# Kernel tuning notes

Hardware: AMD Instinct MI355X
Metric: run time of the kernel (lower is better)

Reference implementation:

```python
import jax, jax.numpy as jnp
import numpy as np


def _maxpool2(x):
    # 2x2 max pool, stride 2, NCHW
    return jax.lax.reduce_window(x, -jnp.inf, jax.lax.max, (1, 1, 2, 2), (1, 1, 2, 2), 'VALID')


def _up2(x):
    # bilinear upsample x2 with align_corners=True (matches nn.Upsample), NCHW, separable
    def rs(a, axis):
        n = a.shape[axis]
        out = 2 * n
        c = jnp.arange(out) * ((n - 1) / (out - 1))
        i0 = jnp.floor(c).astype(jnp.int32)
        i1 = jnp.minimum(i0 + 1, n - 1)
        w = (c - i0).astype(a.dtype)
        lo = jnp.take(a, i0, axis=axis)
        hi = jnp.take(a, i1, axis=axis)
        shp = [1] * a.ndim
        shp[axis] = out
        w = w.reshape(shp)
        return lo * (1 - w) + hi * w
    return rs(rs(x, 2), 3)


def _conv_experts(x, w, b):
    # x [B,Cin,H,W], w [E,Cout,Cin,3,3], b [E,Cout] -> [E,B,Cout,H,W]
    def one(we, be):
        y = jax.lax.conv_general_dilated(x, we, (1, 1), 'SAME',
                                         dimension_numbers=('NCHW', 'OIHW', 'NCHW'))
        return jax.nn.relu(y + be[None, :, None, None])
    return jax.vmap(one)(w, b)


def _moe(x, cw, cb, gw, gb, nw, nb, eps, k):
    # noisy top-k gate (create_gate) + fused gated expert sum (eval_gate)
    B = x.shape[0]
    xf = x.reshape(B, -1)
    g = xf @ gw + gb                      # [B,E]
    noise = jax.nn.softplus(xf @ nw + nb)
    g = g + eps[None, :] * noise          # shared per-expert gaussian noise * per-sample scale
    E = g.shape[1]
    if E > 2:
        _, idx = jax.lax.top_k(g.sum(axis=0), k)   # top-k experts by batch-summed gate
        mask = jnp.zeros((E,), bool).at[idx].set(True)
        g = jnp.where(mask[None, :], g, 0.0)       # zero BEFORE softmax, as in the original
    gate = jax.nn.softmax(g, axis=-1)
    y = _conv_experts(x, cw, cb)          # [E,B,C,H,W]
    # collapses the original experts x batch python double-loop into one contraction
    return jnp.einsum('ebchw,be->bchw', y, gate)


def setup_inputs():
    key = jax.random.key(0)
    keys = iter(jax.random.split(key, 40))
    def rn(shape, scale=1.0):
        return jax.random.normal(next(keys), shape, jnp.float32) * scale
    B, W, E = 2048, 10, 4
    inp = {'x': rn((B, 1, 28, 28))}
    conv_shapes = [(E, W, 1, 3, 3), (E, W, W, 3, 3), (E, 2 * W, W, 3, 3),
                   (E, W, 3 * W, 3, 3), (E, W, 2 * W, 3, 3)]
    gate_in = [784, 1960, 490, 5880, 15680]
    for i in range(5):
        inp[f'cw{i+1}'] = rn(conv_shapes[i], 0.1)
        inp[f'cb{i+1}'] = rn((E, conv_shapes[i][1]), 0.1)
        inp[f'gw{i+1}'] = rn((gate_in[i], E), 0.02)
        inp[f'gb{i+1}'] = rn((E,), 0.02)
        inp[f'nw{i+1}'] = rn((gate_in[i], E), 0.02)
        inp[f'nb{i+1}'] = rn((E,), 0.02)
        inp[f'eps{i+1}'] = rn((E,), 1.0)   # N(mu=0, sigma=1) gate noise, fixed for determinism
    inp['wlast'] = rn((1, W, 1, 1), 0.1)
    inp['blast'] = rn((1,), 0.1)
    inp['k'] = 2
    return inp


def reference(x, cw1, cb1, gw1, gb1, nw1, nb1, eps1,
              cw2, cb2, gw2, gb2, nw2, nb2, eps2,
              cw3, cb3, gw3, gb3, nw3, nb3, eps3,
              cw4, cb4, gw4, gb4, nw4, nb4, eps4,
              cw5, cb5, gw5, gb5, nw5, nb5, eps5,
              wlast, blast, k):
    conv1 = _moe(x, cw1, cb1, gw1, gb1, nw1, nb1, eps1, k)        # [B,10,28,28]
    h = _maxpool2(conv1)                                          # [B,10,14,14]
    conv2 = _moe(h, cw2, cb2, gw2, gb2, nw2, nb2, eps2, k)        # [B,10,14,14]
    h = _maxpool2(conv2)                                          # [B,10,7,7]
    conv3 = _moe(h, cw3, cb3, gw3, gb3, nw3, nb3, eps3, k)        # [B,20,7,7]
    h = jnp.concatenate([_up2(conv3), conv2], axis=1)             # [B,30,14,14]
    h = _moe(h, cw4, cb4, gw4, gb4, nw4, nb4, eps4, k)            # [B,10,14,14]
    h = jnp.concatenate([_up2(h), conv1], axis=1)                 # [B,20,28,28]
    h = _moe(h, cw5, cb5, gw5, gb5, nw5, nb5, eps5, k)            # [B,10,28,28]
    out = jnp.einsum('bchw,oc->bohw', h, wlast[:, :, 0, 0]) + blast[None, :, None, None]
    return out
```

## Files before the change

### kernel.cpp

```cpp
#include <hip/hip_runtime.h>
#include <hip/hip_bf16.h>
#include <math.h>


constexpr int BATCH = 2048;

constexpr size_t PADF    = 1024;
constexpr size_t F_CONV1 = (size_t)BATCH * 10 * 784;
constexpr size_t F_XPAD  = (size_t)BATCH * 784;
constexpr size_t F_P1    = (size_t)BATCH * 10 * 196;
constexpr size_t F_CONV2 = F_P1;
constexpr size_t F_P2    = (size_t)BATCH * 10 * 49;
constexpr size_t F_CONV3 = (size_t)BATCH * 20 * 49;
constexpr size_t F_UP3   = (size_t)BATCH * 20 * 196;
constexpr size_t F_M4    = F_P1;
constexpr size_t F_UP4   = F_CONV1;

constexpr size_t O_CONV1 = PADF;
constexpr size_t O_Z2    = O_CONV1 + F_CONV1 + PADF;
constexpr size_t O_XPAD  = O_Z2;
constexpr size_t O_P1    = O_XPAD + F_XPAD + PADF;
constexpr size_t O_CONV2 = O_P1 + F_P1 + PADF;
constexpr size_t O_P2    = O_CONV2 + F_CONV2 + PADF;
constexpr size_t O_CONV3 = O_P2 + F_P2 + PADF;
constexpr size_t O_UP3   = O_CONV3 + F_CONV3 + PADF;
constexpr size_t O_M4    = O_UP3 + F_UP3 + PADF;
constexpr size_t O_UP4   = O_Z2;
constexpr size_t O_GRAW  = O_M4 + F_M4 + PADF;
constexpr size_t O_CS    = O_GRAW + 5 * (size_t)BATCH * 4;
constexpr size_t WS_FLOATS = O_CS + 5 * 64 + PADF;

__device__ __forceinline__ float softplusf(float z) {
    return fmaxf(z, 0.0f) + log1pf(expf(-fabsf(z)));
}

__device__ __forceinline__ float4 ld4(const float* p) {
    return *(const float4*)p;
}

constexpr int cdivc(int a, int b) { return (a + b - 1) / b; }
constexpr int pb4(int H, int W) {
    return cdivc(BATCH * ((H + 3) / 4) * W, 256);
}

template <int C1HW, int C2HW>
__global__ __launch_bounds__(256) void gate_block_v4(
    const float* __restrict__ x1, const float* __restrict__ x2,
    const float* __restrict__ gw, const float* __restrict__ gb,
    const float* __restrict__ nw, const float* __restrict__ nb,
    const float* __restrict__ eps,
    float* __restrict__ graw)
{
    constexpr int DV = (C1HW + C2HW) / 4;
    const int b   = blockIdx.x;
    const int tid = threadIdx.x;

    float ga0 = 0.f, ga1 = 0.f, ga2 = 0.f, ga3 = 0.f;
    float na0 = 0.f, na1 = 0.f, na2 = 0.f, na3 = 0.f;

    for (int g = tid; g < DV; g += 256) {
        const int d = g * 4;
        float4 xv;
        if constexpr (C2HW > 0) {
            xv = (d < C1HW) ? ld4(x1 + (size_t)b * C1HW + d)
                            : ld4(x2 + (size_t)b * C2HW + (d - C1HW));
        } else {
            xv = ld4(x1 + (size_t)b * C1HW + d);
        }
        const float xs[4] = {xv.x, xv.y, xv.z, xv.w};
        #pragma unroll
        for (int j = 0; j < 4; ++j) {
            const float val = xs[j];
            const float4 gv = ((const float4*)gw)[d + j];
            const float4 nv = ((const float4*)nw)[d + j];
            ga0 = fmaf(val, gv.x, ga0); ga1 = fmaf(val, gv.y, ga1);
            ga2 = fmaf(val, gv.z, ga2); ga3 = fmaf(val, gv.w, ga3);
            na0 = fmaf(val, nv.x, na0); na1 = fmaf(val, nv.y, na1);
            na2 = fmaf(val, nv.z, na2); na3 = fmaf(val, nv.w, na3);
        }
    }
    #pragma unroll
    for (int m = 32; m >= 1; m >>= 1) {
        ga0 += __shfl_xor(ga0, m, 64); ga1 += __shfl_xor(ga1, m, 64);
        ga2 += __shfl_xor(ga2, m, 64); ga3 += __shfl_xor(ga3, m, 64);
        na0 += __shfl_xor(na0, m, 64); na1 += __shfl_xor(na1, m, 64);
        na2 += __shfl_xor(na2, m, 64); na3 += __shfl_xor(na3, m, 64);
    }
    __shared__ float red[4][8];
    const int wave = tid >> 6, lane = tid & 63;
    if (lane == 0) {
        red[wave][0] = ga0; red[wave][1] = ga1; red[wave][2] = ga2; red[wave][3] = ga3;
        red[wave][4] = na0; red[wave][5] = na1; red[wave][6] = na2; red[wave][7] = na3;
    }
    __syncthreads();
    if (tid == 0) {
        float G[8];
        #pragma unroll
        for (int i = 0; i < 8; ++i)
            G[i] = red[0][i] + red[1][i] + red[2][i] + red[3][i];
        #pragma unroll
        for (int e = 0; e < 4; ++e) {
            graw[b * 4 + e] = G[e] + gb[e] + eps[e] * softplusf(G[4 + e] + nb[e]);
        }
    }
}

template <int D>
__global__ __launch_bounds__(256) void gate_block_s(
    const float* __restrict__ x1,
    const float* __restrict__ gw, const float* __restrict__ gb,
    const float* __restrict__ nw, const float* __restrict__ nb,
    const float* __restrict__ eps,
    float* __restrict__ graw)
{
    const int b   = blockIdx.x;
    const int tid = threadIdx.x;

    float ga0 = 0.f, ga1 = 0.f, ga2 = 0.f, ga3 = 0.f;
    float na0 = 0.f, na1 = 0.f, na2 = 0.f, na3 = 0.f;

    for (int d = tid; d < D; d += 256) {
        const float val = x1[(size_t)b * D + d];
        const float4 gv = ((const float4*)gw)[d];
        const float4 nv = ((const float4*)nw)[d];
        ga0 = fmaf(val, gv.x, ga0); ga1 = fmaf(val, gv.y, ga1);
        ga2 = fmaf(val, gv.z, ga2); ga3 = fmaf(val, gv.w, ga3);
        na0 = fmaf(val, nv.x, na0); na1 = fmaf(val, nv.y, na1);
        na2 = fmaf(val, nv.z, na2); na3 = fmaf(val, nv.w, na3);
    }
    #pragma unroll
    for (int m = 32; m >= 1; m >>= 1) {
        ga0 += __shfl_xor(ga0, m, 64); ga1 += __shfl_xor(ga1, m, 64);
        ga2 += __shfl_xor(ga2, m, 64); ga3 += __shfl_xor(ga3, m, 64);
        na0 += __shfl_xor(na0, m, 64); na1 += __shfl_xor(na1, m, 64);
        na2 += __shfl_xor(na2, m, 64); na3 += __shfl_xor(na3, m, 64);
    }
    __shared__ float red[4][8];
    const int wave = tid >> 6, lane = tid & 63;
    if (lane == 0) {
        red[wave][0] = ga0; red[wave][1] = ga1; red[wave][2] = ga2; red[wave][3] = ga3;
        red[wave][4] = na0; red[wave][5] = na1; red[wave][6] = na2; red[wave][7] = na3;
    }
    __syncthreads();
    if (tid == 0) {
        float G[8];
        #pragma unroll
        for (int i = 0; i < 8; ++i)
            G[i] = red[0][i] + red[1][i] + red[2][i] + red[3][i];
        #pragma unroll
        for (int e = 0; e < 4; ++e) {
            graw[b * 4 + e] = G[e] + gb[e] + eps[e] * softplusf(G[4 + e] + nb[e]);
        }
    }
}

__global__ __launch_bounds__(256) void gate_reduce(
    const float* __restrict__ graw, float* __restrict__ cs)
{
    const int tid = threadIdx.x;
    float a0 = 0.f, a1 = 0.f, a2 = 0.f, a3 = 0.f;
    for (int b = tid; b < BATCH; b += 256) {
        const float4 v = ld4(graw + b * 4);
        a0 += v.x; a1 += v.y; a2 += v.z; a3 += v.w;
    }
    #pragma unroll
    for (int m = 32; m >= 1; m >>= 1) {
        a0 += __shfl_xor(a0, m, 64); a1 += __shfl_xor(a1, m, 64);
        a2 += __shfl_xor(a2, m, 64); a3 += __shfl_xor(a3, m, 64);
    }
    __shared__ float red[4][4];
    const int wave = tid >> 6, lane = tid & 63;
    if (lane == 0) {
        red[wave][0] = a0; red[wave][1] = a1; red[wave][2] = a2; red[wave][3] = a3;
    }
    __syncthreads();
    if (tid < 4) {
        cs[tid] = red[0][tid] + red[1][tid] + red[2][tid] + red[3][tid];
    }
}

template <int CIN1, int CIN2, int COUT, int H, int W, int POOL, int FINAL>
__global__ __launch_bounds__(256) void moe_conv4(
    const float* __restrict__ x1, const float* __restrict__ x2,
    const float* __restrict__ cw, const float* __restrict__ cb,
    const float* __restrict__ graw, const float* __restrict__ colsum,
    const int* __restrict__ kp,
    float* __restrict__ out, float* __restrict__ pout,
    const float* __restrict__ wl, const float* __restrict__ bl)
{
    constexpr int CIN = CIN1 + CIN2;
    constexpr int CG  = 2;
    constexpr int NCG = COUT / CG;
    constexpr int HG  = (H + 3) / 4;
    constexpr int TOTAL = BATCH * HG * W;

    __shared__ __align__(16) float wlds[CIN * 72];

    const unsigned bid = blockIdx.x;
    const unsigned xcd = bid & 7u;
    const unsigned sub = bid >> 3;
    const unsigned cg  = sub % NCG;
    const unsigned tl  = sub / NCG;
    const unsigned tile = tl * 8u + xcd;
    const int c0 = (int)cg * CG;

    for (int idx = threadIdx.x; idx < CIN * 72; idx += 256) {
        const int ci = idx / 72;
        const int r  = idx % 72;
        const int k  = r / 8;
        const int je = r % 8;
        wlds[idx] = cw[((size_t)((je & 3) * COUT + c0 + (je >> 2)) * CIN + ci) * 9 + k];
    }
    __syncthreads();

    const int t = (int)tile * 256 + (int)threadIdx.x;
    if (t >= TOTAL) return;
    const int b  = t / (HG * W);
    const int r  = t - b * (HG * W);
    const int hg = r / W;
    const int w  = r - hg * W;
    const int h0 = hg * 4;

    float gt[4];
    {
        int k = kp[0];
        k = (k < 1) ? 1 : (k > 4 ? 4 : k);
        float cs[4], gr[4];
        bool sel[4] = {false, false, false, false};
        #pragma unroll
        for (int e = 0; e < 4; ++e) { cs[e] = colsum[e]; gr[e] = graw[b * 4 + e]; }
        for (int it = 0; it < k; ++it) {
            int bi = 0; float bv = -INFINITY;
            #pragma unroll
            for (int e = 0; e < 4; ++e)
                if (!sel[e] && cs[e] > bv) { bv = cs[e]; bi = e; }
            sel[bi] = true;
        }
        float g[4];
        #pragma unroll
        for (int e = 0; e < 4; ++e) g[e] = sel[e] ? gr[e] : 0.0f;
        const float mx = fmaxf(fmaxf(g[0], g[1]), fmaxf(g[2], g[3]));
        const float e0 = expf(g[0] - mx), e1 = expf(g[1] - mx);
        const float e2 = expf(g[2] - mx), e3 = expf(g[3] - mx);
        const float inv = 1.0f / (e0 + e1 + e2 + e3);
        gt[0] = e0 * inv; gt[1] = e1 * inv; gt[2] = e2 * inv; gt[3] = e3 * inv;
    }

    float m[6][3];
    #pragma unroll
    for (int rr = 0; rr < 6; ++rr) {
        const int y = h0 - 1 + rr;
        const float my = (y >= 0 && y < H) ? 1.0f : 0.0f;
        #pragma unroll
        for (int dc = 0; dc < 3; ++dc) {
            const int xx = w - 1 + dc;
            m[rr][dc] = ((xx >= 0 && xx < W) ? 1.0f : 0.0f) * my;
        }
    }
    const int base = (h0 - 1) * W + (w - 1);

    float acc[4][CG][4];
    #pragma unroll
    for (int j = 0; j < CG; ++j) {
        #pragma unroll
        for (int e = 0; e < 4; ++e) {
            const float bv = cb[e * COUT + c0 + j];
            #pragma unroll
            for (int rr = 0; rr < 4; ++rr) acc[rr][j][e] = bv;
        }
    }

    const float* xb1 = x1 + (size_t)b * CIN1 * (H * W);
    const float* xb2 = (CIN2 > 0) ? (x2 + (size_t)b * CIN2 * (H * W)) : nullptr;

    auto xplane = [&](int ci) -> const float* {
        if constexpr (CIN2 > 0)
            return (ci < CIN1) ? (xb1 + ci * (H * W)) : (xb2 + (ci - CIN1) * (H * W));
        else
            return xb1 + ci * (H * W);
    };
    auto load_taps = [&](int ci, float v[6][3]) {
        const float* xp = xplane(ci);
        #pragma unroll
        for (int rr = 0; rr < 6; ++rr)
            #pragma unroll
            for (int dc = 0; dc < 3; ++dc)
                v[rr][dc] = xp[base + rr * W + dc];
    };
    auto fma_taps = [&](int ci, const float v[6][3]) {
        float mv[6][3];
        #pragma unroll
        for (int rr = 0; rr < 6; ++rr)
            #pragma unroll
            for (int dc = 0; dc < 3; ++dc)
                mv[rr][dc] = v[rr][dc] * m[rr][dc];
        const float4* wp = (const float4*)&wlds[ci * 72];
        #pragma unroll
        for (int k = 0; k < 9; ++k) {
            const float4 wA = wp[k * 2];
            const float4 wB = wp[k * 2 + 1];
            const int kh = k / 3, kw = k % 3;
            #pragma unroll
            for (int rr = 0; rr < 4; ++rr) {
                const float tap = mv[rr + kh][kw];
                acc[rr][0][0] = fmaf(tap, wA.x, acc[rr][0][0]);
                acc[rr][0][1] = fmaf(tap, wA.y, acc[rr][0][1]);
                acc[rr][0][2] = fmaf(tap, wA.z, acc[rr][0][2]);
                acc[rr][0][3] = fmaf(tap, wA.w, acc[rr][0][3]);
                acc[rr][1][0] = fmaf(tap, wB.x, acc[rr][1][0]);
                acc[rr][1][1] = fmaf(tap, wB.y, acc[rr][1][1]);
                acc[rr][1][2] = fmaf(tap, wB.z, acc[rr][1][2]);
                acc[rr][1][3] = fmaf(tap, wB.w, acc[rr][1][3]);
            }
        }
    };

    float vA[6][3], vB[6][3];
    load_taps(0, vA);
    #pragma unroll 1
    for (int ci = 0; ci + 2 <= CIN; ci += 2) {
        load_taps(ci + 1, vB);
        fma_taps(ci, vA);
        if (ci + 2 < CIN) load_taps(ci + 2, vA);
        fma_taps(ci + 1, vB);
    }
    if constexpr (CIN & 1) {
        fma_taps(CIN - 1, vA);
    }

    float s[4][CG];
    #pragma unroll
    for (int rr = 0; rr < 4; ++rr)
        #pragma unroll
        for (int j = 0; j < CG; ++j)
            s[rr][j] = gt[0] * fmaxf(acc[rr][j][0], 0.f)
                     + gt[1] * fmaxf(acc[rr][j][1], 0.f)
                     + gt[2] * fmaxf(acc[rr][j][2], 0.f)
                     + gt[3] * fmaxf(acc[rr][j][3], 0.f);

    if constexpr (FINAL) {
        const float w0 = wl[c0], w1 = wl[c0 + 1];
        const float bshare = bl[0] * (1.0f / (float)NCG);
        float* op = out + (size_t)b * (H * W) + h0 * W + w;
        #pragma unroll
        for (int rr = 0; rr < 4; ++rr) {
            if (h0 + rr < H)
                atomicAdd(&op[rr * W], s[rr][0] * w0 + s[rr][1] * w1 + bshare);
        }
    } else {
        #pragma unroll
        for (int j = 0; j < CG; ++j) {
            float* op = out + ((size_t)b * COUT + c0 + j) * (H * W) + h0 * W + w;
            #pragma unroll
            for (int rr = 0; rr < 4; ++rr)
                if (h0 + rr < H) op[rr * W] = s[rr][j];
        }
    }

    if constexpr (POOL) {
        constexpr int H2 = H / 2, W2 = W / 2;
        #pragma unroll
        for (int j = 0; j < CG; ++j) {
            float cm0 = fmaxf(s[0][j], s[1][j]);
            float cm1 = fmaxf(s[2][j], s[3][j]);
            const float o0 = fmaxf(cm0, __shfl_xor(cm0, 1, 64));
            const float o1 = fmaxf(cm1, __shfl_xor(cm1, 1, 64));
            if ((w & 1) == 0) {
                const int pr0 = h0 >> 1;
                float* pp = pout + ((size_t)b * COUT + c0 + j) * (H2 * W2) + (w >> 1);
                if (pr0     < H2) pp[pr0 * W2]       = o0;
                if (pr0 + 1 < H2) pp[(pr0 + 1) * W2] = o1;
            }
        }
    }
}

template <int N>
__global__ __launch_bounds__(256) void upsample2(
    const float* __restrict__ in, float* __restrict__ out, int BC)
{
    constexpr int M = 2 * N;
    const int idx = blockIdx.x * 256 + threadIdx.x;
    const int total = BC * M * M;
    if (idx >= total) return;
    const int x = idx % M;
    int tmp = idx / M;
    const int y = tmp % M;
    const int bc = tmp / M;
    const float scale = (float)((double)(N - 1) / (double)(M - 1));
    const float cy = (float)y * scale;
    const float cx = (float)x * scale;
    const int iy0 = (int)floorf(cy);
    const int ix0 = (int)floorf(cx);
    const int iy1 = min(iy0 + 1, N - 1);
    const int ix1 = min(ix0 + 1, N - 1);
    const float wy = cy - (float)iy0;
    const float wx = cx - (float)ix0;
    const float* p = in + (size_t)bc * N * N;
    const float v00 = p[iy0 * N + ix0], v01 = p[iy0 * N + ix1];
    const float v10 = p[iy1 * N + ix0], v11 = p[iy1 * N + ix1];
    const float a0 = v00 * (1.0f - wy) + v10 * wy;
    const float a1 = v01 * (1.0f - wy) + v11 * wy;
    out[idx] = a0 * (1.0f - wx) + a1 * wx;
}

extern "C" void kernel_launch(void* const* d_in, const int* in_sizes, int n_in,
                              void* d_out, int out_size, void* d_ws, size_t ws_size,
                              hipStream_t stream)
{
    const float* x = (const float*)d_in[0];
    const float* cw[5]; const float* cb[5]; const float* gw[5]; const float* gb[5];
    const float* nw[5]; const float* nb[5]; const float* epsv[5];
    for (int l = 0; l < 5; ++l) {
        cw[l]   = (const float*)d_in[1 + 7 * l + 0];
        cb[l]   = (const float*)d_in[1 + 7 * l + 1];
        gw[l]   = (const float*)d_in[1 + 7 * l + 2];
        gb[l]   = (const float*)d_in[1 + 7 * l + 3];
        nw[l]   = (const float*)d_in[1 + 7 * l + 4];
        nb[l]   = (const float*)d_in[1 + 7 * l + 5];
        epsv[l] = (const float*)d_in[1 + 7 * l + 6];
    }
    const float* wlast = (const float*)d_in[36];
    const float* blast = (const float*)d_in[37];
    const int*   kp    = (const int*)d_in[38];
    float* out = (float*)d_out;
    float* ws  = (float*)d_ws;

    float* conv1 = ws + O_CONV1;
    float* xpad  = ws + O_XPAD;
    float* p1    = ws + O_P1;
    float* conv2 = ws + O_CONV2;
    float* p2    = ws + O_P2;
    float* conv3 = ws + O_CONV3;
    float* up3   = ws + O_UP3;
    float* m4    = ws + O_M4;
    float* up4   = ws + O_UP4;
    float* graw[5]; float* cs[5];
    for (int l = 0; l < 5; ++l) {
        graw[l] = ws + O_GRAW + (size_t)l * BATCH * 4;
        cs[l]   = ws + O_CS + (size_t)l * 64;
    }

    hipMemsetAsync(out, 0, (size_t)out_size * sizeof(float), stream);
    hipMemcpyAsync(xpad, x, (size_t)BATCH * 784 * sizeof(float),
                   hipMemcpyDeviceToDevice, stream);

    #define CDIV(a) (((a) + 255) / 256)
    const int g1 = pb4(28, 28) * 5;
    const int g2 = pb4(14, 14) * 5;
    const int g3 = pb4(7, 7)   * 10;
    const int g4 = pb4(14, 14) * 5;
    const int g5 = pb4(28, 28) * 5;

    gate_block_v4<784, 0><<<BATCH, 256, 0, stream>>>(
        x, nullptr, gw[0], gb[0], nw[0], nb[0], epsv[0], graw[0]);
    gate_reduce<<<1, 256, 0, stream>>>(graw[0], cs[0]);
    moe_conv4<1, 0, 10, 28, 28, 1, 0><<<g1, 256, 0, stream>>>(
        xpad, nullptr, cw[0], cb[0], graw[0], cs[0], kp, conv1, p1,
        nullptr, nullptr);

    gate_block_v4<1960, 0><<<BATCH, 256, 0, stream>>>(
        p1, nullptr, gw[1], gb[1], nw[1], nb[1], epsv[1], graw[1]);
    gate_reduce<<<1, 256, 0, stream>>>(graw[1], cs[1]);
    moe_conv4<10, 0, 10, 14, 14, 1, 0><<<g2, 256, 0, stream>>>(
        p1, nullptr, cw[1], cb[1], graw[1], cs[1], kp, conv2, p2,
        nullptr, nullptr);

    gate_block_s<490><<<BATCH, 256, 0, stream>>>(
        p2, gw[2], gb[2], nw[2], nb[2], epsv[2], graw[2]);
    gate_reduce<<<1, 256, 0, stream>>>(graw[2], cs[2]);
    moe_conv4<10, 0, 20, 7, 7, 0, 0><<<g3, 256, 0, stream>>>(
        p2, nullptr, cw[2], cb[2], graw[2], cs[2], kp, conv3, nullptr,
        nullptr, nullptr);
    upsample2<7><<<CDIV(BATCH * 20 * 196), 256, 0, stream>>>(conv3, up3, BATCH * 20);

    gate_block_v4<3920, 1960><<<BATCH, 256, 0, stream>>>(
        up3, conv2, gw[3], gb[3], nw[3], nb[3], epsv[3], graw[3]);
    gate_reduce<<<1, 256, 0, stream>>>(graw[3], cs[3]);
    moe_conv4<20, 10, 10, 14, 14, 0, 0><<<g4, 256, 0, stream>>>(
        up3, conv2, cw[3], cb[3], graw[3], cs[3], kp, m4, nullptr,
        nullptr, nullptr);
    upsample2<14><<<CDIV(BATCH * 10 * 784), 256, 0, stream>>>(m4, up4, BATCH * 10);

    gate_block_v4<7840, 7840><<<BATCH, 256, 0, stream>>>(
        up4, conv1, gw[4], gb[4], nw[4], nb[4], epsv[4], graw[4]);
    gate_reduce<<<1, 256, 0, stream>>>(graw[4], cs[4]);
    moe_conv4<10, 10, 10, 28, 28, 0, 1><<<g5, 256, 0, stream>>>(
        up4, conv1, cw[4], cb[4], graw[4], cs[4], kp, out, nullptr,
        wlast, blast);
    #undef CDIV
}
```

Baseline: 871.3 us.

## Add 2x4 register-tiled conv kernel for 28x28 layers and two-sample gate blocks

Adds a new moe_conv_q4 kernel for the 28x28 layers (conv1 and conv5). Each thread computes a 2-row by 4-column output patch from vectorized float4 row loads, double-buffers input channels, and writes results and the fused 2x2 pool as float4/float2 stores. The old kernel had each thread compute a 4x1 column. The gate GEMV blocks now process two samples per block so the gw/nw weight loads are shared, and the launch grid is halved. The new tile relies on the xpad/workspace padding for out-of-range halo reads and uses more registers, which may lower occupancy.

Measured after the change: 829.2 us. -4.8%, faster.

```diff
diff --git a/kernel.cpp b/kernel.cpp
--- a/kernel.cpp
+++ b/kernel.cpp
@@ -52,55 +52,73 @@
     float* __restrict__ graw)
 {
     constexpr int DV = (C1HW + C2HW) / 4;
-    const int b   = blockIdx.x;
+    const int b0  = blockIdx.x * 2;
     const int tid = threadIdx.x;
 
-    float ga0 = 0.f, ga1 = 0.f, ga2 = 0.f, ga3 = 0.f;
-    float na0 = 0.f, na1 = 0.f, na2 = 0.f, na3 = 0.f;
+    float ga[2][4] = {}, na[2][4] = {};
 
     for (int g = tid; g < DV; g += 256) {
         const int d = g * 4;
-        float4 xv;
-        if constexpr (C2HW > 0) {
-            xv = (d < C1HW) ? ld4(x1 + (size_t)b * C1HW + d)
-                            : ld4(x2 + (size_t)b * C2HW + (d - C1HW));
-        } else {
-            xv = ld4(x1 + (size_t)b * C1HW + d);
-        }
-        const float xs[4] = {xv.x, xv.y, xv.z, xv.w};
+        float4 xv[2];
+        #pragma unroll
+        for (int ss = 0; ss < 2; ++ss) {
+            const int b = b0 + ss;
+            if constexpr (C2HW > 0) {
+                xv[ss] = (d < C1HW) ? ld4(x1 + (size_t)b * C1HW + d)
+                                    : ld4(x2 + (size_t)b * C2HW + (d - C1HW));
+            } else {
+                xv[ss] = ld4(x1 + (size_t)b * C1HW + d);
+            }
+        }
         #pragma unroll
         for (int j = 0; j < 4; ++j) {
-            const float val = xs[j];
             const float4 gv = ((const float4*)gw)[d + j];
             const float4 nv = ((const float4*)nw)[d + j];
-            ga0 = fmaf(val, gv.x, ga0); ga1 = fmaf(val, gv.y, ga1);
-            ga2 = fmaf(val, gv.z, ga2); ga3 = fmaf(val, gv.w, ga3);
-            na0 = fmaf(val, nv.x, na0); na1 = fmaf(val, nv.y, na1);
-            na2 = fmaf(val, nv.z, na2); na3 = fmaf(val, nv.w, na3);
+            #pragma unroll
+            for (int ss = 0; ss < 2; ++ss) {
+                const float val = (&xv[ss].x)[j];
+                ga[ss][0] = fmaf(val, gv.x, ga[ss][0]);
+                ga[ss][1] = fmaf(val, gv.y, ga[ss][1]);
+                ga[ss][2] = fmaf(val, gv.z, ga[ss][2]);
+                ga[ss][3] = fmaf(val, gv.w, ga[ss][3]);
+                na[ss][0] = fmaf(val, nv.x, na[ss][0]);
+                na[ss][1] = fmaf(val, nv.y, na[ss][1]);
+                na[ss][2] = fmaf(val, nv.z, na[ss][2]);
+                na[ss][3] = fmaf(val, nv.w, na[ss][3]);
+            }
         }
     }
     #pragma unroll
     for (int m = 32; m >= 1; m >>= 1) {
-        ga0 += __shfl_xor(ga0, m, 64); ga1 += __shfl_xor(ga1, m, 64);
-        ga2 += __shfl_xor(ga2, m, 64); ga3 += __shfl_xor(ga3, m, 64);
-        na0 += __shfl_xor(na0, m, 64); na1 += __shfl_xor(na1, m, 64);
-        na2 += __shfl_xor(na2, m, 64); na3 += __shfl_xor(na3, m, 64);
-    }
-    __shared__ float red[4][8];
+        #pragma unroll
+        for (int ss = 0; ss < 2; ++ss)
+            #pragma unroll
+            for (int e = 0; e < 4; ++e) {
+                ga[ss][e] += __shfl_xor(ga[ss][e], m, 64);
+                na[ss][e] += __shfl_xor(na[ss][e], m, 64);
+            }
+    }
+    __shared__ float red[4][16];
     const int wave = tid >> 6, lane = tid & 63;
     if (lane == 0) {
-        red[wave][0] = ga0; red[wave][1] = ga1; red[wave][2] = ga2; red[wave][3] = ga3;
-        red[wave][4] = na0; red[wave][5] = na1; red[wave][6] = na2; red[wave][7] = na3;
+        #pragma unroll
+        for (int ss = 0; ss < 2; ++ss)
+            #pragma unroll
+            for (int e = 0; e < 4; ++e) {
+                red[wave][ss * 8 + e]     = ga[ss][e];
+                red[wave][ss * 8 + 4 + e] = na[ss][e];
+            }
     }
     __syncthreads();
-    if (tid == 0) {
-        float G[8];
-        #pragma unroll
-        for (int i = 0; i < 8; ++i)
-            G[i] = red[0][i] + red[1][i] + red[2][i] + red[3][i];
+    if (tid < 2) {
+        const int ss = tid;
         #pragma unroll
         for (int e = 0; e < 4; ++e) {
-            graw[b * 4 + e] = G[e] + gb[e] + eps[e] * softplusf(G[4 + e] + nb[e]);
+            const float G = red[0][ss*8+e] + red[1][ss*8+e]
+                          + red[2][ss*8+e] + red[3][ss*8+e];
+            const float N = red[0][ss*8+4+e] + red[1][ss*8+4+e]
+                          + red[2][ss*8+4+e] + red[3][ss*8+4+e];
+            graw[(b0 + ss) * 4 + e] = G + gb[e] + eps[e] * softplusf(N + nb[e]);
         }
     }
 }
@@ -179,8 +197,35 @@
     }
 }
 
-template <int CIN1, int CIN2, int COUT, int H, int W, int POOL, int FINAL>
-__global__ __launch_bounds__(256) void moe_conv4(
+__device__ __forceinline__ void gate_final(
+    const float* __restrict__ graw, const float* __restrict__ colsum,
+    const int* __restrict__ kp, int b, float gt[4])
+{
+    float cs[4], gr[4];
+    #pragma unroll
+    for (int e = 0; e < 4; ++e) { cs[e] = colsum[e]; gr[e] = graw[b * 4 + e]; }
+    int k = kp[0];
+    k = (k < 1) ? 1 : (k > 4 ? 4 : k);
+    bool sel[4] = {false, false, false, false};
+    for (int it = 0; it < k; ++it) {
+        int bi = 0; float bv = -INFINITY;
+        #pragma unroll
+        for (int e = 0; e < 4; ++e)
+            if (!sel[e] && cs[e] > bv) { bv = cs[e]; bi = e; }
+        sel[bi] = true;
+    }
+    float g[4];
+    #pragma unroll
+    for (int e = 0; e < 4; ++e) g[e] = sel[e] ? gr[e] : 0.0f;
+    const float mx = fmaxf(fmaxf(g[0], g[1]), fmaxf(g[2], g[3]));
+    const float e0 = expf(g[0] - mx), e1 = expf(g[1] - mx);
+    const float e2 = expf(g[2] - mx), e3 = expf(g[3] - mx);
+    const float inv = 1.0f / (e0 + e1 + e2 + e3);
+    gt[0] = e0 * inv; gt[1] = e1 * inv; gt[2] = e2 * inv; gt[3] = e3 * inv;
+}
+
+template <int CIN1, int CIN2, int COUT, int POOL, int FINAL>
+__global__ __launch_bounds__(256) void moe_conv_q4(
     const float* __restrict__ x1, const float* __restrict__ x2,
     const float* __restrict__ cw, const float* __restrict__ cb,
     const float* __restrict__ graw, const float* __restrict__ colsum,
@@ -188,11 +233,11 @@
     float* __restrict__ out, float* __restrict__ pout,
     const float* __restrict__ wl, const float* __restrict__ bl)
 {
+    constexpr int H = 28, W = 28;
     constexpr int CIN = CIN1 + CIN2;
     constexpr int CG  = 2;
     constexpr int NCG = COUT / CG;
-    constexpr int HG  = (H + 3) / 4;
-    constexpr int TOTAL = BATCH * HG * W;
+    constexpr int TOTAL = BATCH * 14 * 7;
 
     __shared__ __align__(16) float wlds[CIN * 72];
 
@@ -215,6 +260,186 @@
 
     const int t = (int)tile * 256 + (int)threadIdx.x;
     if (t >= TOTAL) return;
+    const int b  = t / 98;
+    const int r  = t - b * 98;
+    const int hh = r / 7;
+    const int q  = r - hh * 7;
+    const int h0 = 2 * hh;
+    const int w0 = 4 * q;
+
+    float gt[4];
+    gate_final(graw, colsum, kp, b, gt);
+
+    const float rt = (h0 > 0)      ? 1.0f : 0.0f;
+    const float rb = (h0 + 2 < H)  ? 1.0f : 0.0f;
+    const float cl = (w0 > 0)      ? 1.0f : 0.0f;
+    const float cr = (w0 + 4 < W)  ? 1.0f : 0.0f;
+
+    float acc[2][4][CG][4];
+    #pragma unroll
+    for (int j = 0; j < CG; ++j) {
+        #pragma unroll
+        for (int e = 0; e < 4; ++e) {
+            const float bv = cb[e * COUT + c0 + j];
+            #pragma unroll
+            for (int rr = 0; rr < 2; ++rr)
+                #pragma unroll
+                for (int p = 0; p < 4; ++p) acc[rr][p][j][e] = bv;
+        }
+    }
+
+    const int rbase = (h0 - 1) * W + w0;
+    const float* xb1 = x1 + (size_t)b * CIN1 * (H * W);
+    const float* xb2 = (CIN2 > 0) ? (x2 + (size_t)b * CIN2 * (H * W)) : nullptr;
+
+    auto xplane = [&](int ci) -> const float* {
+        if constexpr (CIN2 > 0)
+            return (ci < CIN1) ? (xb1 + ci * (H * W)) : (xb2 + (ci - CIN1) * (H * W));
+        else
+            return xb1 + ci * (H * W);
+    };
+    auto load_taps = [&](int ci, float v[4][6]) {
+        const float* rp = xplane(ci) + rbase;
+        #pragma unroll
+        for (int rr = 0; rr < 4; ++rr) {
+            const float4 c = ld4(rp + rr * W);
+            v[rr][0] = rp[rr * W - 1];
+            v[rr][1] = c.x; v[rr][2] = c.y; v[rr][3] = c.z; v[rr][4] = c.w;
+            v[rr][5] = rp[rr * W + 4];
+        }
+    };
+    auto fma_taps = [&](int ci, const float v[4][6]) {
+        float mv[4][6];
+        #pragma unroll
+        for (int rr = 0; rr < 4; ++rr) {
+            #pragma unroll
+            for (int c = 0; c < 6; ++c) mv[rr][c] = v[rr][c];
+            mv[rr][0] *= cl;
+            mv[rr][5] *= cr;
+        }
+        #pragma unroll
+        for (int c = 0; c < 6; ++c) { mv[0][c] *= rt; mv[3][c] *= rb; }
+
+        const float4* wp = (const float4*)&wlds[ci * 72];
+        #pragma unroll
+        for (int k = 0; k < 9; ++k) {
+            const float4 wA = wp[k * 2];
+            const float4 wB = wp[k * 2 + 1];
+            const int kh = k / 3, kw = k % 3;
+            #pragma unroll
+            for (int rr = 0; rr < 2; ++rr) {
+                #pragma unroll
+                for (int p = 0; p < 4; ++p) {
+                    const float tap = mv[rr + kh][p + kw];
+                    acc[rr][p][0][0] = fmaf(tap, wA.x, acc[rr][p][0][0]);
+                    acc[rr][p][0][1] = fmaf(tap, wA.y, acc[rr][p][0][1]);
+                    acc[rr][p][0][2] = fmaf(tap, wA.z, acc[rr][p][0][2]);
+                    acc[rr][p][0][3] = fmaf(tap, wA.w, acc[rr][p][0][3]);
+                    acc[rr][p][1][0] = fmaf(tap, wB.x, acc[rr][p][1][0]);
+                    acc[rr][p][1][1] = fmaf(tap, wB.y, acc[rr][p][1][1]);
+                    acc[rr][p][1][2] = fmaf(tap, wB.z, acc[rr][p][1][2]);
+                    acc[rr][p][1][3] = fmaf(tap, wB.w, acc[rr][p][1][3]);
+                }
+            }
+        }
+    };
+
+    float vA[4][6], vB[4][6];
+    load_taps(0, vA);
+    #pragma unroll 1
+    for (int ci = 0; ci + 2 <= CIN; ci += 2) {
+        load_taps(ci + 1, vB);
+        fma_taps(ci, vA);
+        if (ci + 2 < CIN) load_taps(ci + 2, vA);
+        fma_taps(ci + 1, vB);
+    }
+    if constexpr (CIN & 1) {
+        fma_taps(CIN - 1, vA);
+    }
+
+    float s[2][4][CG];
+    #pragma unroll
+    for (int rr = 0; rr < 2; ++rr)
+        #pragma unroll
+        for (int p = 0; p < 4; ++p)
+            #pragma unroll
+            for (int j = 0; j < CG; ++j)
+                s[rr][p][j] = gt[0] * fmaxf(acc[rr][p][j][0], 0.f)
+                            + gt[1] * fmaxf(acc[rr][p][j][1], 0.f)
+                            + gt[2] * fmaxf(acc[rr][p][j][2], 0.f)
+                            + gt[3] * fmaxf(acc[rr][p][j][3], 0.f);
+
+    if constexpr (FINAL) {
+        const float w0f = wl[c0], w1f = wl[c0 + 1];
+        const float bshare = bl[0] * (1.0f / (float)NCG);
+        float* op = out + (size_t)b * (H * W) + h0 * W + w0;
+        #pragma unroll
+        for (int rr = 0; rr < 2; ++rr)
+            #pragma unroll
+            for (int p = 0; p < 4; ++p)
+                atomicAdd(&op[rr * W + p],
+                          s[rr][p][0] * w0f + s[rr][p][1] * w1f + bshare);
+    } else {
+        #pragma unroll
+        for (int j = 0; j < CG; ++j) {
+            float* op = out + ((size_t)b * COUT + c0 + j) * (H * W) + h0 * W + w0;
+            #pragma unroll
+            for (int rr = 0; rr < 2; ++rr) {
+                float4 o = {s[rr][0][j], s[rr][1][j], s[rr][2][j], s[rr][3][j]};
+                *(float4*)(op + rr * W) = o;
+            }
+        }
+    }
+
+    if constexpr (POOL) {
+        constexpr int H2 = 14, W2 = 14;
+        #pragma unroll
+        for (int j = 0; j < CG; ++j) {
+            float2 o;
+            o.x = fmaxf(fmaxf(s[0][0][j], s[0][1][j]), fmaxf(s[1][0][j], s[1][1][j]));
+            o.y = fmaxf(fmaxf(s[0][2][j], s[0][3][j]), fmaxf(s[1][2][j], s[1][3][j]));
+            float* pp = pout + ((size_t)b * COUT + c0 + j) * (H2 * W2)
+                        + hh * W2 + (w0 >> 1);
+            *(float2*)pp = o;
+        }
+    }
+}
+
+template <int CIN1, int CIN2, int COUT, int H, int W, int POOL>
+__global__ __launch_bounds__(256) void moe_conv4(
+    const float* __restrict__ x1, const float* __restrict__ x2,
+    const float* __restrict__ cw, const float* __restrict__ cb,
+    const float* __restrict__ graw, const float* __restrict__ colsum,
+    const int* __restrict__ kp,
+    float* __restrict__ out, float* __restrict__ pout)
+{
+    constexpr int CIN = CIN1 + CIN2;
+    constexpr int CG  = 2;
+    constexpr int NCG = COUT / CG;
+    constexpr int HG  = (H + 3) / 4;
+    constexpr int TOTAL = BATCH * HG * W;
+
+    __shared__ __align__(16) float wlds[CIN * 72];
+
+    const unsigned bid = blockIdx.x;
+    const unsigned xcd = bid & 7u;
+    const unsigned sub = bid >> 3;
+    const unsigned cg  = sub % NCG;
+    const unsigned tl  = sub / NCG;
+    const unsigned tile = tl * 8u + xcd;
+    const int c0 = (int)cg * CG;
+
+    for (int idx = threadIdx.x; idx < CIN * 72; idx += 256) {
+        const int ci = idx / 72;
+        const int r  = idx % 72;
+        const int k  = r / 8;
+        const int je = r % 8;
+        wlds[idx] = cw[((size_t)((je & 3) * COUT + c0 + (je >> 2)) * CIN + ci) * 9 + k];
+    }
+    __syncthreads();
+
+    const int t = (int)tile * 256 + (int)threadIdx.x;
+    if (t >= TOTAL) return;
     const int b  = t / (HG * W);
     const int r  = t - b * (HG * W);
     const int hg = r / W;
@@ -222,29 +447,7 @@
     const int h0 = hg * 4;
 
     float gt[4];
-    {
-        int k = kp[0];
-        k = (k < 1) ? 1 : (k > 4 ? 4 : k);
-        float cs[4], gr[4];
-        bool sel[4] = {false, false, false, false};
-        #pragma unroll
-        for (int e = 0; e < 4; ++e) { cs[e] = colsum[e]; gr[e] = graw[b * 4 + e]; }
-        for (int it = 0; it < k; ++it) {
-            int bi = 0; float bv = -INFINITY;
-            #pragma unroll
-            for (int e = 0; e < 4; ++e)
-                if (!sel[e] && cs[e] > bv) { bv = cs[e]; bi = e; }
-            sel[bi] = true;
-        }
-        float g[4];
-        #pragma unroll
-        for (int e = 0; e < 4; ++e) g[e] = sel[e] ? gr[e] : 0.0f;
-        const float mx = fmaxf(fmaxf(g[0], g[1]), fmaxf(g[2], g[3]));
-        const float e0 = expf(g[0] - mx), e1 = expf(g[1] - mx);
-        const float e2 = expf(g[2] - mx), e3 = expf(g[3] - mx);
-        const float inv = 1.0f / (e0 + e1 + e2 + e3);
-        gt[0] = e0 * inv; gt[1] = e1 * inv; gt[2] = e2 * inv; gt[3] = e3 * inv;
-    }
+    gate_final(graw, colsum, kp, b, gt);
 
     float m[6][3];
     #pragma unroll
@@ -338,23 +541,12 @@
                      + gt[2] * fmaxf(acc[rr][j][2], 0.f)
                      + gt[3] * fmaxf(acc[rr][j][3], 0.f);
 
-    if constexpr (FINAL) {
-        const float w0 = wl[c0], w1 = wl[c0 + 1];
-        const float bshare = bl[0] * (1.0f / (float)NCG);
-        float* op = out + (size_t)b * (H * W) + h0 * W + w;
-        #pragma unroll
-        for (int rr = 0; rr < 4; ++rr) {
-            if (h0 + rr < H)
-                atomicAdd(&op[rr * W], s[rr][0] * w0 + s[rr][1] * w1 + bshare);
-        }
-    } else {
-        #pragma unroll
-        for (int j = 0; j < CG; ++j) {
-            float* op = out + ((size_t)b * COUT + c0 + j) * (H * W) + h0 * W + w;
-            #pragma unroll
-            for (int rr = 0; rr < 4; ++rr)
-                if (h0 + rr < H) op[rr * W] = s[rr][j];
-        }
+    #pragma unroll
+    for (int j = 0; j < CG; ++j) {
+        float* op = out + ((size_t)b * COUT + c0 + j) * (H * W) + h0 * W + w;
+        #pragma unroll
+        for (int rr = 0; rr < 4; ++rr)
+            if (h0 + rr < H) op[rr * W] = s[rr][j];
     }
 
     if constexpr (POOL) {
@@ -446,46 +638,43 @@
                    hipMemcpyDeviceToDevice, stream);
 
     #define CDIV(a) (((a) + 255) / 256)
-    const int g1 = pb4(28, 28) * 5;
-    const int g2 = pb4(14, 14) * 5;
-    const int g3 = pb4(7, 7)   * 10;
-    const int g4 = pb4(14, 14) * 5;
-    const int g5 = pb4(28, 28) * 5;
-
-    gate_block_v4<784, 0><<<BATCH, 256, 0, stream>>>(
+    const int gq  = 784 * 5;
+    const int g2  = pb4(14, 14) * 5;
+    const int g3  = pb4(7, 7)   * 10;
+    const int g4  = pb4(14, 14) * 5;
+    const int GB2 = BATCH / 2;
+
+    gate_block_v4<784, 0><<<GB2, 256, 0, stream>>>(
         x, nullptr, gw[0], gb[0], nw[0], nb[0], epsv[0], graw[0]);
     gate_reduce<<<1, 256, 0, stream>>>(graw[0], cs[0]);
-    moe_conv4<1, 0, 10, 28, 28, 1, 0><<<g1, 256, 0, stream>>>(
+    moe_conv_q4<1, 0, 10, 1, 0><<<gq, 256, 0, stream>>>(
         xpad, nullptr, cw[0], cb[0], graw[0], cs[0], kp, conv1, p1,
         nullptr, nullptr);
 
-    gate_block_v4<1960, 0><<<BATCH, 256, 0, stream>>>(
+    gate_block_v4<1960, 0><<<GB2, 256, 0, stream>>>(
         p1, nullptr, gw[1], gb[1], nw[1], nb[1], epsv[1], graw[1]);
     gate_reduce<<<1, 256, 0, stream>>>(graw[1], cs[1]);
-    moe_conv4<10, 0, 10, 14, 14, 1, 0><<<g2, 256, 0, stream>>>(
-        p1, nullptr, cw[1], cb[1], graw[1], cs[1], kp, conv2, p2,
-        nullptr, nullptr);
+    moe_conv4<10, 0, 10, 14, 14, 1><<<g2, 256, 0, stream>>>(
+        p1, nullptr, cw[1], cb[1], graw[1], cs[1], kp, conv2, p2);
 
     gate_block_s<490><<<BATCH, 256, 0, stream>>>(
         p2, gw[2], gb[2], nw[2], nb[2], epsv[2], graw[2]);
     gate_reduce<<<1, 256, 0, stream>>>(graw[2], cs[2]);
-    moe_conv4<10, 0, 20, 7, 7, 0, 0><<<g3, 256, 0, stream>>>(
-        p2, nullptr, cw[2], cb[2], graw[2], cs[2], kp, conv3, nullptr,
-        nullptr, nullptr);
+    moe_conv4<10, 0, 20, 7, 7, 0><<<g3, 256, 0, stream>>>(
+        p2, nullptr, cw[2], cb[2], graw[2], cs[2], kp, conv3, nullptr);
     upsample2<7><<<CDIV(BATCH * 20 * 196), 256, 0, stream>>>(conv3, up3, BATCH * 20);
 
-    gate_block_v4<3920, 1960><<<BATCH, 256, 0, stream>>>(
+    gate_block_v4<3920, 1960><<<GB2, 256, 0, stream>>>(
         up3, conv2, gw[3], gb[3], nw[3], nb[3], epsv[3], graw[3]);
     gate_reduce<<<1, 256, 0, stream>>>(graw[3], cs[3]);
-    moe_conv4<20, 10, 10, 14, 14, 0, 0><<<g4, 256, 0, stream>>>(
-        up3, conv2, cw[3], cb[3], graw[3], cs[3], kp, m4, nullptr,
-        nullptr, nullptr);
+    moe_conv4<20, 10, 10, 14, 14, 0><<<g4, 256, 0, stream>>>(
+        up3, conv2, cw[3], cb[3], graw[3], cs[3], kp, m4, nullptr);
     upsample2<14><<<CDIV(BATCH * 10 * 784), 256, 0, stream>>>(m4, up4, BATCH * 10);
 
-    gate_block_v4<7840, 7840><<<BATCH, 256, 0, stream>>>(
+    gate_block_v4<7840, 7840><<<GB2, 256, 0, stream>>>(
         up4, conv1, gw[4], gb[4], nw[4], nb[4], epsv[4], graw[4]);
     gate_reduce<<<1, 256, 0, stream>>>(graw[4], cs[4]);
-    moe_conv4<10, 10, 10, 28, 28, 0, 1><<<g5, 256, 0, stream>>>(
+    moe_conv_q4<10, 10, 10, 0, 1><<<gq, 256, 0, stream>>>(
         up4, conv1, cw[4], cb[4], graw[4], cs[4], kp, out, nullptr,
         wlast, blast);
     #undef CDIV
```
